# Optimization experiments

Hardware: AMD Instinct MI355X
Metric: run time of the kernel (lower is better)

The kernel has to match this reference:

```python
import jax, jax.numpy as jnp
import numpy as np

B, S_CTX, S_Q, D_CTX, D_Q = 16, 2048, 2048, 1024, 1024
MASK_P = 0.1  # fraction of masked context positions


def setup_inputs() -> dict:
    key = jax.random.key(0)
    k1, k2, k3, k4 = jax.random.split(key, 4)
    context = jax.random.normal(k1, (B, S_CTX, D_CTX), dtype=jnp.float32)
    query = jax.random.normal(k2, (S_Q, B, D_Q), dtype=jnp.float32)  # [q_steps, batch, query_size]
    W = jax.random.normal(k3, (D_CTX, D_Q), dtype=jnp.float32)       # learned bilinear weights
    context_mask = jax.random.uniform(k4, (B, S_CTX)) < MASK_P       # True = masked position
    return {"context": context, "query": query, "W": W, "context_mask": context_mask}


def reference(context, query, W, context_mask):
    # scores[b, q, s] = context[b, s, :] @ W @ query[q, b, :]   (temp = 1.0, so no scaling)
    cw = jnp.einsum('bsd,de->bse', context, W)            # [B, S_ctx, D_q]
    scores = jnp.einsum('bse,qbe->bqs', cw, query)        # [B, S_q, S_ctx]
    neg = jnp.asarray(-1e30, scores.dtype)                # finite stand-in for -inf (NaN-safe)
    scores = jnp.where(context_mask[:, None, :], neg, scores)
    attn = jax.nn.softmax(scores, axis=2)                 # [B, S_q, S_ctx]
    # rows where the whole context is masked get attention zeroed out
    all_masked = jnp.all(context_mask, axis=1)[:, None, None]
    attn = jnp.where(all_masked, jnp.asarray(0.0, attn.dtype), attn)
    composition = jnp.einsum('bqs,bsd->qbd', attn, context)  # [S_q, B, D_ctx]
    attn_out = attn.transpose(1, 0, 2)                       # [S_q, B, S_ctx]
    return attn_out, composition
```

## Files before the change

kernel.cpp:

```cpp
#include <hip/hip_runtime.h>
#include <cmath>

#define B_  16
#define SEQ 2048
#define DIM 1024
#define LDST 40

typedef short  short8 __attribute__((ext_vector_type(8)));
typedef short  sh4    __attribute__((ext_vector_type(4)));
typedef float  f32x4  __attribute__((ext_vector_type(4)));

__device__ __forceinline__ unsigned short f2bf(float x) {
  unsigned u = __builtin_bit_cast(unsigned, x);
  return (unsigned short)((u + 0x7fffu + ((u >> 16) & 1u)) >> 16);
}
__device__ __forceinline__ float bf2f(unsigned short h) {
  unsigned u = ((unsigned)h) << 16;
  return __builtin_bit_cast(float, u);
}

__device__ __forceinline__ void gl16(const void* g, void* l) {
  __builtin_amdgcn_global_load_lds(
      (const __attribute__((address_space(1))) void*)g,
      (__attribute__((address_space(3))) void*)l, 16, 0, 0);
}

__global__ __launch_bounds__(256) void cvt_ctx(const float* __restrict__ X,
                                               unsigned short* __restrict__ hi,
                                               unsigned short* __restrict__ lo) {
  const size_t N8 = (size_t)B_ * SEQ * DIM / 8;
  for (size_t i = (size_t)blockIdx.x * 256 + threadIdx.x; i < N8;
       i += (size_t)gridDim.x * 256) {
    const size_t base = i * 8;
    float4 a = *(const float4*)&X[base];
    float4 c = *(const float4*)&X[base + 4];
    const float xs[8] = {a.x, a.y, a.z, a.w, c.x, c.y, c.z, c.w};
    short8 h, l;
#pragma unroll
    for (int j = 0; j < 8; ++j) {
      unsigned short hh = f2bf(xs[j]);
      h[j] = (short)hh;
      l[j] = (short)f2bf(xs[j] - bf2f(hh));
    }
    *(short8*)&hi[base] = h;
    *(short8*)&lo[base] = l;
  }
}

__global__ __launch_bounds__(256) void t_ctx(const float* __restrict__ X,
                                             unsigned short* __restrict__ T) {
  __shared__ unsigned short L[64 * 72];
  const int t = threadIdx.x;
  const int d0 = blockIdx.x * 64, s0 = blockIdx.y * 64, b = blockIdx.z;
#pragma unroll
  for (int p = 0; p < 4; ++p) {
    const int sl = (t >> 4) + p * 16, d4 = (t & 15) * 4;
    float4 v = *(const float4*)&X[((size_t)b * SEQ + s0 + sl) * DIM + d0 + d4];
    sh4 o = {(short)f2bf(v.x), (short)f2bf(v.y), (short)f2bf(v.z), (short)f2bf(v.w)};
    *(sh4*)&L[sl * 72 + d4] = o;
  }
  __syncthreads();
#pragma unroll
  for (int p = 0; p < 4; ++p) {
    const int dl = (t >> 4) + p * 16, s4 = (t & 15) * 4;
    sh4 o = {(short)L[(s4 + 0) * 72 + dl], (short)L[(s4 + 1) * 72 + dl],
             (short)L[(s4 + 2) * 72 + dl], (short)L[(s4 + 3) * 72 + dl]};
    *(sh4*)&T[((size_t)b * DIM + d0 + dl) * SEQ + s0 + s4] = o;
  }
}

__global__ __launch_bounds__(256) void g1_z(const float* __restrict__ Q,
                                            const float* __restrict__ W,
                                            unsigned short* __restrict__ zhi,
                                            unsigned short* __restrict__ zlo) {
  __shared__ unsigned short Ah[128 * LDST], Al[128 * LDST];
  __shared__ unsigned short Bh[128 * LDST], Bl[128 * LDST];
  const int tid = threadIdx.x;
  const int m0 = blockIdx.y * 128, n0 = blockIdx.x * 128;
  const int wave = tid >> 6, lane = tid & 63;
  const int wm = (wave >> 1) * 64, wn = (wave & 1) * 64;
  const int rl = tid & 127;

  const float* srow = (tid < 128) ? Q + (size_t)(m0 + rl) * DIM
                                  : W + (size_t)(n0 + rl) * DIM;
  unsigned short* th = (tid < 128) ? Ah : Bh;
  unsigned short* tl = (tid < 128) ? Al : Bl;

  f32x4 acc[4][4];
#pragma unroll
  for (int i = 0; i < 4; ++i)
#pragma unroll
    for (int j = 0; j < 4; ++j) acc[i][j] = (f32x4){0.f, 0.f, 0.f, 0.f};

  for (int kc = 0; kc < DIM; kc += 32) {
    float4 fv[8];
#pragma unroll
    for (int j = 0; j < 8; ++j) fv[j] = *(const float4*)&srow[kc + j * 4];
    __syncthreads();
    short8 hv[4], lv[4];
#pragma unroll
    for (int j = 0; j < 8; ++j) {
      const float x[4] = {fv[j].x, fv[j].y, fv[j].z, fv[j].w};
#pragma unroll
      for (int c = 0; c < 4; ++c) {
        unsigned short h = f2bf(x[c]);
        unsigned short l = f2bf(x[c] - bf2f(h));
        hv[j >> 1][(j & 1) * 4 + c] = (short)h;
        lv[j >> 1][(j & 1) * 4 + c] = (short)l;
      }
    }
#pragma unroll
    for (int j = 0; j < 4; ++j) {
      *(short8*)&th[rl * LDST + j * 8] = hv[j];
      *(short8*)&tl[rl * LDST + j * 8] = lv[j];
    }
    __syncthreads();

    short8 ah[4], al[4], bh[4], bl[4];
#pragma unroll
    for (int f = 0; f < 4; ++f) {
      const int ao = (wm + f * 16 + (lane & 15)) * LDST + (lane >> 4) * 8;
      const int bo = (wn + f * 16 + (lane & 15)) * LDST + (lane >> 4) * 8;
      ah[f] = *(const short8*)&Ah[ao];  al[f] = *(const short8*)&Al[ao];
      bh[f] = *(const short8*)&Bh[bo];  bl[f] = *(const short8*)&Bl[bo];
    }
#pragma unroll
    for (int i = 0; i < 4; ++i)
#pragma unroll
      for (int j = 0; j < 4; ++j) {
        acc[i][j] = __builtin_amdgcn_mfma_f32_16x16x32_bf16(ah[i], bh[j], acc[i][j], 0, 0, 0);
        acc[i][j] = __builtin_amdgcn_mfma_f32_16x16x32_bf16(al[i], bh[j], acc[i][j], 0, 0, 0);
        acc[i][j] = __builtin_amdgcn_mfma_f32_16x16x32_bf16(ah[i], bl[j], acc[i][j], 0, 0, 0);
      }
  }
#pragma unroll
  for (int i = 0; i < 4; ++i)
#pragma unroll
    for (int j = 0; j < 4; ++j)
#pragma unroll
      for (int r = 0; r < 4; ++r) {
        const int row = m0 + wm + i * 16 + (lane >> 4) * 4 + r;
        const int col = n0 + wn + j * 16 + (lane & 15);
        const float v = acc[i][j][r];
        const unsigned short h = f2bf(v);
        zhi[(size_t)row * DIM + col] = h;
        zlo[(size_t)row * DIM + col] = f2bf(v - bf2f(h));
      }
}

#define G2GRID (16 * 16 * B_)
__global__ __launch_bounds__(256) void g2_scores(const unsigned short* __restrict__ zhi,
                                                 const unsigned short* __restrict__ zlo,
                                                 const unsigned short* __restrict__ chi,
                                                 const unsigned short* __restrict__ clo,
                                                 float* __restrict__ Sc) {
  __shared__ unsigned short Sh[128 * 32], Sl[128 * 32];
  __shared__ unsigned short Qh[128 * 32], Ql[128 * 32];
  const int tid = threadIdx.x, lane = tid & 63, wave = tid >> 6;

  const int lin = blockIdx.x;
  const int swz = (lin & 7) * (G2GRID / 8) + (lin >> 3);
  const int s0 = (swz & 15) * 128;
  const int q0 = ((swz >> 4) & 15) * 128;
  const int b  = swz >> 8;

  const int wm = (wave >> 1) * 64;
  const int wn = (wave & 1) * 64;

  const int r_sub = lane >> 2;
  const int c_sub = (((lane & 3) ^ ((lane >> 3) & 3))) * 8;

  f32x4 acc[4][4];
#pragma unroll
  for (int i = 0; i < 4; ++i)
#pragma unroll
    for (int j = 0; j < 4; ++j) acc[i][j] = (f32x4){0.f, 0.f, 0.f, 0.f};

  for (int kc = 0; kc < DIM; kc += 32) {
    if (wave == 0) {
#pragma unroll
      for (int it = 0; it < 8; ++it)
        gl16(&chi[((size_t)b * SEQ + s0 + it * 16 + r_sub) * DIM + kc + c_sub], &Sh[it * 512]);
    } else if (wave == 1) {
#pragma unroll
      for (int it = 0; it < 8; ++it)
        gl16(&clo[((size_t)b * SEQ + s0 + it * 16 + r_sub) * DIM + kc + c_sub], &Sl[it * 512]);
    } else if (wave == 2) {
#pragma unroll
      for (int it = 0; it < 8; ++it)
        gl16(&zhi[((size_t)(q0 + it * 16 + r_sub) * B_ + b) * DIM + kc + c_sub], &Qh[it * 512]);
    } else {
#pragma unroll
      for (int it = 0; it < 8; ++it)
        gl16(&zlo[((size_t)(q0 + it * 16 + r_sub) * B_ + b) * DIM + kc + c_sub], &Ql[it * 512]);
    }
    __syncthreads();

    short8 sh_[4], sl_[4], qh_[4], ql_[4];
#pragma unroll
    for (int f = 0; f < 4; ++f) {
      const int ra = wm + f * 16 + (lane & 15);
      const int rb = wn + f * 16 + (lane & 15);
      const int so = ra * 32 + (((lane >> 4) ^ ((ra >> 1) & 3))) * 8;
      const int qo = rb * 32 + (((lane >> 4) ^ ((rb >> 1) & 3))) * 8;
      sh_[f] = *(const short8*)&Sh[so];  sl_[f] = *(const short8*)&Sl[so];
      qh_[f] = *(const short8*)&Qh[qo];  ql_[f] = *(const short8*)&Ql[qo];
    }
#pragma unroll
    for (int i = 0; i < 4; ++i)
#pragma unroll
      for (int j = 0; j < 4; ++j) {
        acc[i][j] = __builtin_amdgcn_mfma_f32_16x16x32_bf16(sh_[i], qh_[j], acc[i][j], 0, 0, 0);
        acc[i][j] = __builtin_amdgcn_mfma_f32_16x16x32_bf16(sl_[i], qh_[j], acc[i][j], 0, 0, 0);
        acc[i][j] = __builtin_amdgcn_mfma_f32_16x16x32_bf16(sh_[i], ql_[j], acc[i][j], 0, 0, 0);
      }
    __syncthreads();
  }

#pragma unroll
  for (int i = 0; i < 4; ++i)
#pragma unroll
    for (int j = 0; j < 4; ++j) {
      const int s = s0 + wm + i * 16 + (lane >> 4) * 4;
      const int q = q0 + wn + j * 16 + (lane & 15);
      f32x4 v = {acc[i][j][0], acc[i][j][1], acc[i][j][2], acc[i][j][3]};
      __builtin_nontemporal_store(v, (f32x4*)&Sc[((size_t)q * B_ + b) * SEQ + s]);
    }
}

__global__ __launch_bounds__(256) void kernel_softmax(float* __restrict__ attn,
                                                      const int* __restrict__ mask) {
  const int row = blockIdx.x;
  const int b = row & (B_ - 1);
  float* p = attn + (size_t)row * SEQ;
  const int* m = mask + (size_t)b * SEQ;
  const int t = threadIdx.x;

  float v[8];
  float mx = -INFINITY;
#pragma unroll
  for (int i = 0; i < 8; ++i) {
    const int s = t + i * 256;
    float x = p[s];
    x = m[s] ? -1e30f : x;
    v[i] = x;
    mx = fmaxf(mx, x);
  }
#pragma unroll
  for (int off = 32; off > 0; off >>= 1) mx = fmaxf(mx, __shfl_xor(mx, off));
  __shared__ float redmax[4];
  __shared__ float redsum[4];
  if ((t & 63) == 0) redmax[t >> 6] = mx;
  __syncthreads();
  mx = fmaxf(fmaxf(redmax[0], redmax[1]), fmaxf(redmax[2], redmax[3]));

  float sum = 0.f;
#pragma unroll
  for (int i = 0; i < 8; ++i) {
    v[i] = __expf(v[i] - mx);
    sum += v[i];
  }
#pragma unroll
  for (int off = 32; off > 0; off >>= 1) sum += __shfl_xor(sum, off);
  if ((t & 63) == 0) redsum[t >> 6] = sum;
  __syncthreads();
  sum = (redsum[0] + redsum[1]) + (redsum[2] + redsum[3]);

  const bool allmasked = (mx < -1e29f);
  const float inv = allmasked ? 0.f : 1.f / sum;
#pragma unroll
  for (int i = 0; i < 8; ++i) p[t + i * 256] = v[i] * inv;
}

__global__ __launch_bounds__(256) void g3_comp(const float* __restrict__ attn,
                                               const unsigned short* __restrict__ ctxT,
                                               float* __restrict__ Out) {
  __shared__ unsigned short Ad[128 * 32];
  __shared__ unsigned short Bq[128 * 32];
  const int tid = threadIdx.x, lane = tid & 63, wave = tid >> 6;
  const int b = blockIdx.z;
  const int d0 = blockIdx.x * 128, q0 = blockIdx.y * 128;
  const int wm = (wave >> 1) * 64;
  const int wn = (wave & 1) * 64;

  const int r_sub = lane >> 2;
  const int c_sub = (((lane & 3) ^ ((lane >> 3) & 3))) * 8;

  const int qrow = tid >> 1, shalf = (tid & 1) * 16;
  const float* arow = attn + ((size_t)(q0 + qrow) * B_ + b) * SEQ;
  const int qsw = (qrow >> 1) & 3;
  const int blk_base = (tid & 1) * 2;
  unsigned short* bdst0 = &Bq[qrow * 32 + ((blk_base + 0) ^ qsw) * 8];
  unsigned short* bdst1 = &Bq[qrow * 32 + ((blk_base + 1) ^ qsw) * 8];

  f32x4 acc[4][4];
#pragma unroll
  for (int i = 0; i < 4; ++i)
#pragma unroll
    for (int j = 0; j < 4; ++j) acc[i][j] = (f32x4){0.f, 0.f, 0.f, 0.f};

  for (int kc = 0; kc < SEQ; kc += 32) {
    float4 fv[4];
#pragma unroll
    for (int j = 0; j < 4; ++j) fv[j] = *(const float4*)&arow[kc + shalf + j * 4];
#pragma unroll
    for (int i = 0; i < 2; ++i) {
      const int rb = wave * 32 + i * 16;
      gl16(&ctxT[((size_t)b * DIM + d0 + rb + r_sub) * SEQ + kc + c_sub], &Ad[rb * 32]);
    }
    short8 bv0, bv1;
#pragma unroll
    for (int j = 0; j < 4; ++j) {
      const float x[4] = {fv[j].x, fv[j].y, fv[j].z, fv[j].w};
#pragma unroll
      for (int c = 0; c < 4; ++c) {
        const int e = j * 4 + c;
        if (e < 8) bv0[e] = (short)f2bf(x[c]);
        else       bv1[e - 8] = (short)f2bf(x[c]);
      }
    }
    *(short8*)bdst0 = bv0;
    *(short8*)bdst1 = bv1;
    __syncthreads();

    short8 af[4], bf_[4];
#pragma unroll
    for (int f = 0; f < 4; ++f) {
      const int ra = wm + f * 16 + (lane & 15);
      const int rb = wn + f * 16 + (lane & 15);
      af[f]  = *(const short8*)&Ad[ra * 32 + (((lane >> 4) ^ ((ra >> 1) & 3))) * 8];
      bf_[f] = *(const short8*)&Bq[rb * 32 + (((lane >> 4) ^ ((rb >> 1) & 3))) * 8];
    }
#pragma unroll
    for (int i = 0; i < 4; ++i)
#pragma unroll
      for (int j = 0; j < 4; ++j)
        acc[i][j] = __builtin_amdgcn_mfma_f32_16x16x32_bf16(af[i], bf_[j], acc[i][j], 0, 0, 0);
    __syncthreads();
  }

#pragma unroll
  for (int i = 0; i < 4; ++i)
#pragma unroll
    for (int j = 0; j < 4; ++j) {
      const int d = d0 + wm + i * 16 + (lane >> 4) * 4;
      const int q = q0 + wn + j * 16 + (lane & 15);
      f32x4 v = {acc[i][j][0], acc[i][j][1], acc[i][j][2], acc[i][j][3]};
      __builtin_nontemporal_store(v, (f32x4*)&Out[((size_t)q * B_ + b) * DIM + d]);
    }
}

extern "C" void kernel_launch(void* const* d_in, const int* in_sizes, int n_in,
                              void* d_out, int out_size, void* d_ws, size_t ws_size,
                              hipStream_t stream) {
  const float* context = (const float*)d_in[0];
  const float* query   = (const float*)d_in[1];
  const float* W       = (const float*)d_in[2];
  const int*   mask    = (const int*)d_in[3];

  float* attn = (float*)d_out;
  float* comp = attn + (size_t)SEQ * B_ * SEQ;

  unsigned short* chi = (unsigned short*)comp;
  unsigned short* clo = chi + (size_t)B_ * SEQ * DIM;

  unsigned short* zhi  = (unsigned short*)d_ws;
  unsigned short* zlo  = zhi + (size_t)SEQ * B_ * DIM;
  unsigned short* ctxT = (unsigned short*)d_ws;

  cvt_ctx<<<dim3(4096), 256, 0, stream>>>(context, chi, clo);
  g1_z<<<dim3(DIM / 128, (SEQ * B_) / 128), 256, 0, stream>>>(query, W, zhi, zlo);
  g2_scores<<<dim3(G2GRID), 256, 0, stream>>>(zhi, zlo, chi, clo, attn);
  t_ctx<<<dim3(DIM / 64, SEQ / 64, B_), 256, 0, stream>>>(context, ctxT);
  kernel_softmax<<<dim3(SEQ * B_), 256, 0, stream>>>(attn, mask);
  g3_comp<<<dim3(DIM / 128, SEQ / 128, B_), 256, 0, stream>>>(attn, ctxT, comp);
}
```

Baseline: 1.258 ms.

## Double-buffer LDS in score and composition GEMMs, vectorize softmax accesses

The g2_scores and g3_comp kernels now use two LDS buffers, so the next K-chunk's global-to-LDS loads (and, in g3_comp, the attention fp32 loads and bf16 conversion) are issued before the MFMAs on the current chunk. This is meant to hide global memory latency behind compute and leaves one barrier per iteration instead of two, with explicit waitcnt and sched_barrier placement. The softmax kernel switches to contiguous float4/int4 loads and stores per thread. The cost is doubled LDS use, which may reduce occupancy, and more hand-managed synchronisation.

```diff
diff --git a/kernel.cpp b/kernel.cpp
--- a/kernel.cpp
+++ b/kernel.cpp
@@ -24,6 +24,11 @@
       (const __attribute__((address_space(1))) void*)g,
       (__attribute__((address_space(3))) void*)l, 16, 0, 0);
 }
+
+#define VMCNT0   asm volatile("s_waitcnt vmcnt(0)" ::: "memory")
+#define LGKMCNT0 asm volatile("s_waitcnt lgkmcnt(0)" ::: "memory")
+#define SCHEDB   __builtin_amdgcn_sched_barrier(0)
+#define SBAR     __builtin_amdgcn_s_barrier()
 
 __global__ __launch_bounds__(256) void cvt_ctx(const float* __restrict__ X,
                                                unsigned short* __restrict__ hi,
@@ -154,8 +159,8 @@
                                                  const unsigned short* __restrict__ chi,
                                                  const unsigned short* __restrict__ clo,
                                                  float* __restrict__ Sc) {
-  __shared__ unsigned short Sh[128 * 32], Sl[128 * 32];
-  __shared__ unsigned short Qh[128 * 32], Ql[128 * 32];
+  __shared__ unsigned short Sh[2][128 * 32], Sl[2][128 * 32];
+  __shared__ unsigned short Qh[2][128 * 32], Ql[2][128 * 32];
   const int tid = threadIdx.x, lane = tid & 63, wave = tid >> 6;
 
   const int lin = blockIdx.x;
@@ -170,32 +175,40 @@
   const int r_sub = lane >> 2;
   const int c_sub = (((lane & 3) ^ ((lane >> 3) & 3))) * 8;
 
+  const unsigned short* plane = (wave == 0) ? chi : (wave == 1) ? clo
+                              : (wave == 2) ? zhi : zlo;
+  const size_t gbase  = (wave < 2) ? ((size_t)b * SEQ + s0) * DIM
+                                   : ((size_t)q0 * B_ + b) * DIM;
+  const size_t gpitch = (wave < 2) ? (size_t)DIM : (size_t)B_ * DIM;
+  const unsigned short* gp = plane + gbase + (size_t)r_sub * gpitch + c_sub;
+  unsigned short* lb[2] = {
+    (wave == 0) ? Sh[0] : (wave == 1) ? Sl[0] : (wave == 2) ? Qh[0] : Ql[0],
+    (wave == 0) ? Sh[1] : (wave == 1) ? Sl[1] : (wave == 2) ? Qh[1] : Ql[1]};
+
+  auto stage = [&](unsigned short* dst, int kc) {
+#pragma unroll
+    for (int it = 0; it < 8; ++it)
+      gl16(gp + (size_t)it * 16 * gpitch + kc, dst + it * 512);
+  };
+
   f32x4 acc[4][4];
 #pragma unroll
   for (int i = 0; i < 4; ++i)
 #pragma unroll
     for (int j = 0; j < 4; ++j) acc[i][j] = (f32x4){0.f, 0.f, 0.f, 0.f};
 
+  stage(lb[0], 0);
+  VMCNT0;
+  SBAR; SCHEDB;
+
+  int cur = 0;
   for (int kc = 0; kc < DIM; kc += 32) {
-    if (wave == 0) {
-#pragma unroll
-      for (int it = 0; it < 8; ++it)
-        gl16(&chi[((size_t)b * SEQ + s0 + it * 16 + r_sub) * DIM + kc + c_sub], &Sh[it * 512]);
-    } else if (wave == 1) {
-#pragma unroll
-      for (int it = 0; it < 8; ++it)
-        gl16(&clo[((size_t)b * SEQ + s0 + it * 16 + r_sub) * DIM + kc + c_sub], &Sl[it * 512]);
-    } else if (wave == 2) {
-#pragma unroll
-      for (int it = 0; it < 8; ++it)
-        gl16(&zhi[((size_t)(q0 + it * 16 + r_sub) * B_ + b) * DIM + kc + c_sub], &Qh[it * 512]);
-    } else {
-#pragma unroll
-      for (int it = 0; it < 8; ++it)
-        gl16(&zlo[((size_t)(q0 + it * 16 + r_sub) * B_ + b) * DIM + kc + c_sub], &Ql[it * 512]);
-    }
-    __syncthreads();
-
+    if (kc + 32 < DIM) stage(lb[cur ^ 1], kc + 32);
+
+    const unsigned short* Shc = Sh[cur];
+    const unsigned short* Slc = Sl[cur];
+    const unsigned short* Qhc = Qh[cur];
+    const unsigned short* Qlc = Ql[cur];
     short8 sh_[4], sl_[4], qh_[4], ql_[4];
 #pragma unroll
     for (int f = 0; f < 4; ++f) {
@@ -203,8 +216,8 @@
       const int rb = wn + f * 16 + (lane & 15);
       const int so = ra * 32 + (((lane >> 4) ^ ((ra >> 1) & 3))) * 8;
       const int qo = rb * 32 + (((lane >> 4) ^ ((rb >> 1) & 3))) * 8;
-      sh_[f] = *(const short8*)&Sh[so];  sl_[f] = *(const short8*)&Sl[so];
-      qh_[f] = *(const short8*)&Qh[qo];  ql_[f] = *(const short8*)&Ql[qo];
+      sh_[f] = *(const short8*)&Shc[so];  sl_[f] = *(const short8*)&Slc[so];
+      qh_[f] = *(const short8*)&Qhc[qo];  ql_[f] = *(const short8*)&Qlc[qo];
     }
 #pragma unroll
     for (int i = 0; i < 4; ++i)
@@ -214,7 +227,9 @@
         acc[i][j] = __builtin_amdgcn_mfma_f32_16x16x32_bf16(sl_[i], qh_[j], acc[i][j], 0, 0, 0);
         acc[i][j] = __builtin_amdgcn_mfma_f32_16x16x32_bf16(sh_[i], ql_[j], acc[i][j], 0, 0, 0);
       }
-    __syncthreads();
+    VMCNT0;
+    SCHEDB; SBAR; SCHEDB;
+    cur ^= 1;
   }
 
 #pragma unroll
@@ -236,16 +251,17 @@
   const int* m = mask + (size_t)b * SEQ;
   const int t = threadIdx.x;
 
-  float v[8];
+  float4 va = *(const float4*)&p[t * 8];
+  float4 vb = *(const float4*)&p[t * 8 + 4];
+  int4 ma = *(const int4*)&m[t * 8];
+  int4 mb = *(const int4*)&m[t * 8 + 4];
+  float v[8] = {ma.x ? -1e30f : va.x, ma.y ? -1e30f : va.y,
+                ma.z ? -1e30f : va.z, ma.w ? -1e30f : va.w,
+                mb.x ? -1e30f : vb.x, mb.y ? -1e30f : vb.y,
+                mb.z ? -1e30f : vb.z, mb.w ? -1e30f : vb.w};
   float mx = -INFINITY;
 #pragma unroll
-  for (int i = 0; i < 8; ++i) {
-    const int s = t + i * 256;
-    float x = p[s];
-    x = m[s] ? -1e30f : x;
-    v[i] = x;
-    mx = fmaxf(mx, x);
-  }
+  for (int i = 0; i < 8; ++i) mx = fmaxf(mx, v[i]);
 #pragma unroll
   for (int off = 32; off > 0; off >>= 1) mx = fmaxf(mx, __shfl_xor(mx, off));
   __shared__ float redmax[4];
@@ -268,15 +284,17 @@
 
   const bool allmasked = (mx < -1e29f);
   const float inv = allmasked ? 0.f : 1.f / sum;
-#pragma unroll
-  for (int i = 0; i < 8; ++i) p[t + i * 256] = v[i] * inv;
+  float4 oa = {v[0] * inv, v[1] * inv, v[2] * inv, v[3] * inv};
+  float4 ob = {v[4] * inv, v[5] * inv, v[6] * inv, v[7] * inv};
+  *(float4*)&p[t * 8] = oa;
+  *(float4*)&p[t * 8 + 4] = ob;
 }
 
 __global__ __launch_bounds__(256) void g3_comp(const float* __restrict__ attn,
                                                const unsigned short* __restrict__ ctxT,
                                                float* __restrict__ Out) {
-  __shared__ unsigned short Ad[128 * 32];
-  __shared__ unsigned short Bq[128 * 32];
+  __shared__ unsigned short Ad[2][128 * 32];
+  __shared__ unsigned short Bq[2][128 * 32];
   const int tid = threadIdx.x, lane = tid & 63, wave = tid >> 6;
   const int b = blockIdx.z;
   const int d0 = blockIdx.x * 128, q0 = blockIdx.y * 128;
@@ -286,12 +304,20 @@
   const int r_sub = lane >> 2;
   const int c_sub = (((lane & 3) ^ ((lane >> 3) & 3))) * 8;
 
+  const unsigned short* agp =
+      ctxT + ((size_t)b * DIM + d0 + wave * 32 + r_sub) * SEQ + c_sub;
+  auto stageA = [&](unsigned short* dst, int kc) {
+#pragma unroll
+    for (int i = 0; i < 2; ++i)
+      gl16(agp + (size_t)i * 16 * SEQ + kc, dst + (wave * 32 + i * 16) * 32);
+  };
+
   const int qrow = tid >> 1, shalf = (tid & 1) * 16;
   const float* arow = attn + ((size_t)(q0 + qrow) * B_ + b) * SEQ;
   const int qsw = (qrow >> 1) & 3;
   const int blk_base = (tid & 1) * 2;
-  unsigned short* bdst0 = &Bq[qrow * 32 + ((blk_base + 0) ^ qsw) * 8];
-  unsigned short* bdst1 = &Bq[qrow * 32 + ((blk_base + 1) ^ qsw) * 8];
+  const int bo0 = qrow * 32 + ((blk_base + 0) ^ qsw) * 8;
+  const int bo1 = qrow * 32 + ((blk_base + 1) ^ qsw) * 8;
 
   f32x4 acc[4][4];
 #pragma unroll
@@ -299,44 +325,75 @@
 #pragma unroll
     for (int j = 0; j < 4; ++j) acc[i][j] = (f32x4){0.f, 0.f, 0.f, 0.f};
 
-  for (int kc = 0; kc < SEQ; kc += 32) {
-    float4 fv[4];
-#pragma unroll
-    for (int j = 0; j < 4; ++j) fv[j] = *(const float4*)&arow[kc + shalf + j * 4];
-#pragma unroll
-    for (int i = 0; i < 2; ++i) {
-      const int rb = wave * 32 + i * 16;
-      gl16(&ctxT[((size_t)b * DIM + d0 + rb + r_sub) * SEQ + kc + c_sub], &Ad[rb * 32]);
-    }
-    short8 bv0, bv1;
+  float4 pv[4];
+#pragma unroll
+  for (int j = 0; j < 4; ++j) pv[j] = *(const float4*)&arow[shalf + j * 4];
+  stageA(Ad[0], 0);
+  VMCNT0;
+  {
+    short8 b0, b1;
 #pragma unroll
     for (int j = 0; j < 4; ++j) {
-      const float x[4] = {fv[j].x, fv[j].y, fv[j].z, fv[j].w};
+      const float x[4] = {pv[j].x, pv[j].y, pv[j].z, pv[j].w};
 #pragma unroll
       for (int c = 0; c < 4; ++c) {
         const int e = j * 4 + c;
-        if (e < 8) bv0[e] = (short)f2bf(x[c]);
-        else       bv1[e - 8] = (short)f2bf(x[c]);
-      }
-    }
-    *(short8*)bdst0 = bv0;
-    *(short8*)bdst1 = bv1;
-    __syncthreads();
-
+        if (e < 8) b0[e] = (short)f2bf(x[c]);
+        else       b1[e - 8] = (short)f2bf(x[c]);
+      }
+    }
+    *(short8*)&Bq[0][bo0] = b0;
+    *(short8*)&Bq[0][bo1] = b1;
+  }
+  LGKMCNT0;
+  SBAR; SCHEDB;
+
+  int cur = 0;
+  for (int kc = 0; kc < SEQ; kc += 32) {
+    const bool more = (kc + 32 < SEQ);
+    float4 nv[4];
+    if (more) {
+#pragma unroll
+      for (int j = 0; j < 4; ++j) nv[j] = *(const float4*)&arow[kc + 32 + shalf + j * 4];
+      stageA(Ad[cur ^ 1], kc + 32);
+    }
+
+    const unsigned short* Adc = Ad[cur];
+    const unsigned short* Bqc = Bq[cur];
     short8 af[4], bf_[4];
 #pragma unroll
     for (int f = 0; f < 4; ++f) {
       const int ra = wm + f * 16 + (lane & 15);
       const int rb = wn + f * 16 + (lane & 15);
-      af[f]  = *(const short8*)&Ad[ra * 32 + (((lane >> 4) ^ ((ra >> 1) & 3))) * 8];
-      bf_[f] = *(const short8*)&Bq[rb * 32 + (((lane >> 4) ^ ((rb >> 1) & 3))) * 8];
+      af[f]  = *(const short8*)&Adc[ra * 32 + (((lane >> 4) ^ ((ra >> 1) & 3))) * 8];
+      bf_[f] = *(const short8*)&Bqc[rb * 32 + (((lane >> 4) ^ ((rb >> 1) & 3))) * 8];
     }
 #pragma unroll
     for (int i = 0; i < 4; ++i)
 #pragma unroll
       for (int j = 0; j < 4; ++j)
         acc[i][j] = __builtin_amdgcn_mfma_f32_16x16x32_bf16(af[i], bf_[j], acc[i][j], 0, 0, 0);
-    __syncthreads();
+
+    VMCNT0;
+    if (more) {
+      short8 b0, b1;
+#pragma unroll
+      for (int j = 0; j < 4; ++j) {
+        const float x[4] = {nv[j].x, nv[j].y, nv[j].z, nv[j].w};
+#pragma unroll
+        for (int c = 0; c < 4; ++c) {
+          const int e = j * 4 + c;
+          if (e < 8) b0[e] = (short)f2bf(x[c]);
+          else       b1[e - 8] = (short)f2bf(x[c]);
+        }
+      }
+      unsigned short* Bqn = Bq[cur ^ 1];
+      *(short8*)&Bqn[bo0] = b0;
+      *(short8*)&Bqn[bo1] = b1;
+    }
+    LGKMCNT0;
+    SCHEDB; SBAR; SCHEDB;
+    cur ^= 1;
   }
 
 #pragma unroll
```

Measured after the change: 1.295 ms. +2.9%, slower.

## Enlarge score and composition GEMM tiles to 256x256 with 8 waves

Applied to the files above, without the earlier changes.

The scores and composition GEMMs move from 128x128 tiles with 4 waves to 256x256 tiles with 8 waves per block. Each wave now computes a 128x64 sub-tile, and the A fragments are loaded per row inside the MFMA loop to hold down register use. The composition grid is linearized and swizzled. The aim is more MFMA work per LDS load and less global traffic per output. The softmax kernel also switches to vectorized float4/int4 loads and stores with contiguous per-thread chunks. The price is higher register pressure (a 32-accumulator array per wave) and fewer, larger blocks, which could hurt occupancy or tail balance.

```diff
diff --git a/kernel.cpp b/kernel.cpp
--- a/kernel.cpp
+++ b/kernel.cpp
@@ -148,77 +148,78 @@
       }
 }
 
-#define G2GRID (16 * 16 * B_)
-__global__ __launch_bounds__(256) void g2_scores(const unsigned short* __restrict__ zhi,
-                                                 const unsigned short* __restrict__ zlo,
-                                                 const unsigned short* __restrict__ chi,
-                                                 const unsigned short* __restrict__ clo,
-                                                 float* __restrict__ Sc) {
-  __shared__ unsigned short Sh[128 * 32], Sl[128 * 32];
-  __shared__ unsigned short Qh[128 * 32], Ql[128 * 32];
+#define G2GRID 1024
+__global__ __launch_bounds__(512, 2) void g2_scores(const unsigned short* __restrict__ zhi,
+                                                    const unsigned short* __restrict__ zlo,
+                                                    const unsigned short* __restrict__ chi,
+                                                    const unsigned short* __restrict__ clo,
+                                                    float* __restrict__ Sc) {
+  __shared__ unsigned short Sh[256 * 32], Sl[256 * 32];
+  __shared__ unsigned short Qh[256 * 32], Ql[256 * 32];
   const int tid = threadIdx.x, lane = tid & 63, wave = tid >> 6;
 
   const int lin = blockIdx.x;
   const int swz = (lin & 7) * (G2GRID / 8) + (lin >> 3);
-  const int s0 = (swz & 15) * 128;
-  const int q0 = ((swz >> 4) & 15) * 128;
-  const int b  = swz >> 8;
-
-  const int wm = (wave >> 1) * 64;
-  const int wn = (wave & 1) * 64;
+  const int b   = swz >> 6;
+  const int tile = swz & 63;
+  const int s0 = (tile >> 3) * 256;
+  const int q0 = (tile & 7) * 256;
+
+  const int wm = (wave >> 2) * 128;
+  const int wn = (wave & 3) * 64;
 
   const int r_sub = lane >> 2;
   const int c_sub = (((lane & 3) ^ ((lane >> 3) & 3))) * 8;
 
-  f32x4 acc[4][4];
-#pragma unroll
-  for (int i = 0; i < 4; ++i)
+  const int plane_id = wave >> 1;
+  const int rowoff   = (wave & 1) * 128;
+  const unsigned short* plane = (plane_id == 0) ? chi : (plane_id == 1) ? clo
+                              : (plane_id == 2) ? zhi : zlo;
+  const size_t gbase  = (plane_id < 2) ? ((size_t)b * SEQ + s0 + rowoff) * DIM
+                                       : ((size_t)(q0 + rowoff) * B_ + b) * DIM;
+  const size_t gpitch = (plane_id < 2) ? (size_t)DIM : (size_t)B_ * DIM;
+  const unsigned short* gp = plane + gbase + (size_t)r_sub * gpitch + c_sub;
+  unsigned short* lbase = ((plane_id == 0) ? Sh : (plane_id == 1) ? Sl
+                         : (plane_id == 2) ? Qh : Ql) + rowoff * 32;
+
+  f32x4 acc[8][4];
+#pragma unroll
+  for (int i = 0; i < 8; ++i)
 #pragma unroll
     for (int j = 0; j < 4; ++j) acc[i][j] = (f32x4){0.f, 0.f, 0.f, 0.f};
 
   for (int kc = 0; kc < DIM; kc += 32) {
-    if (wave == 0) {
-#pragma unroll
-      for (int it = 0; it < 8; ++it)
-        gl16(&chi[((size_t)b * SEQ + s0 + it * 16 + r_sub) * DIM + kc + c_sub], &Sh[it * 512]);
-    } else if (wave == 1) {
-#pragma unroll
-      for (int it = 0; it < 8; ++it)
-        gl16(&clo[((size_t)b * SEQ + s0 + it * 16 + r_sub) * DIM + kc + c_sub], &Sl[it * 512]);
-    } else if (wave == 2) {
-#pragma unroll
-      for (int it = 0; it < 8; ++it)
-        gl16(&zhi[((size_t)(q0 + it * 16 + r_sub) * B_ + b) * DIM + kc + c_sub], &Qh[it * 512]);
-    } else {
-#pragma unroll
-      for (int it = 0; it < 8; ++it)
-        gl16(&zlo[((size_t)(q0 + it * 16 + r_sub) * B_ + b) * DIM + kc + c_sub], &Ql[it * 512]);
-    }
-    __syncthreads();
-
-    short8 sh_[4], sl_[4], qh_[4], ql_[4];
-#pragma unroll
-    for (int f = 0; f < 4; ++f) {
-      const int ra = wm + f * 16 + (lane & 15);
-      const int rb = wn + f * 16 + (lane & 15);
+#pragma unroll
+    for (int it = 0; it < 8; ++it)
+      gl16(gp + (size_t)it * 16 * gpitch + kc, lbase + it * 512);
+    __syncthreads();
+
+    short8 qh_[4], ql_[4];
+#pragma unroll
+    for (int j = 0; j < 4; ++j) {
+      const int rb = wn + j * 16 + (lane & 15);
+      const int qo = rb * 32 + (((lane >> 4) ^ ((rb >> 1) & 3))) * 8;
+      qh_[j] = *(const short8*)&Qh[qo];
+      ql_[j] = *(const short8*)&Ql[qo];
+    }
+#pragma unroll
+    for (int i = 0; i < 8; ++i) {
+      const int ra = wm + i * 16 + (lane & 15);
       const int so = ra * 32 + (((lane >> 4) ^ ((ra >> 1) & 3))) * 8;
-      const int qo = rb * 32 + (((lane >> 4) ^ ((rb >> 1) & 3))) * 8;
-      sh_[f] = *(const short8*)&Sh[so];  sl_[f] = *(const short8*)&Sl[so];
-      qh_[f] = *(const short8*)&Qh[qo];  ql_[f] = *(const short8*)&Ql[qo];
-    }
-#pragma unroll
-    for (int i = 0; i < 4; ++i)
+      const short8 shf = *(const short8*)&Sh[so];
+      const short8 slf = *(const short8*)&Sl[so];
 #pragma unroll
       for (int j = 0; j < 4; ++j) {
-        acc[i][j] = __builtin_amdgcn_mfma_f32_16x16x32_bf16(sh_[i], qh_[j], acc[i][j], 0, 0, 0);
-        acc[i][j] = __builtin_amdgcn_mfma_f32_16x16x32_bf16(sl_[i], qh_[j], acc[i][j], 0, 0, 0);
-        acc[i][j] = __builtin_amdgcn_mfma_f32_16x16x32_bf16(sh_[i], ql_[j], acc[i][j], 0, 0, 0);
-      }
-    __syncthreads();
-  }
-
-#pragma unroll
-  for (int i = 0; i < 4; ++i)
+        acc[i][j] = __builtin_amdgcn_mfma_f32_16x16x32_bf16(shf, qh_[j], acc[i][j], 0, 0, 0);
+        acc[i][j] = __builtin_amdgcn_mfma_f32_16x16x32_bf16(slf, qh_[j], acc[i][j], 0, 0, 0);
+        acc[i][j] = __builtin_amdgcn_mfma_f32_16x16x32_bf16(shf, ql_[j], acc[i][j], 0, 0, 0);
+      }
+    }
+    __syncthreads();
+  }
+
+#pragma unroll
+  for (int i = 0; i < 8; ++i)
 #pragma unroll
     for (int j = 0; j < 4; ++j) {
       const int s = s0 + wm + i * 16 + (lane >> 4) * 4;
@@ -236,16 +237,17 @@
   const int* m = mask + (size_t)b * SEQ;
   const int t = threadIdx.x;
 
-  float v[8];
+  float4 va = *(const float4*)&p[t * 8];
+  float4 vb = *(const float4*)&p[t * 8 + 4];
+  int4 ma = *(const int4*)&m[t * 8];
+  int4 mb = *(const int4*)&m[t * 8 + 4];
+  float v[8] = {ma.x ? -1e30f : va.x, ma.y ? -1e30f : va.y,
+                ma.z ? -1e30f : va.z, ma.w ? -1e30f : va.w,
+                mb.x ? -1e30f : vb.x, mb.y ? -1e30f : vb.y,
+                mb.z ? -1e30f : vb.z, mb.w ? -1e30f : vb.w};
   float mx = -INFINITY;
 #pragma unroll
-  for (int i = 0; i < 8; ++i) {
-    const int s = t + i * 256;
-    float x = p[s];
-    x = m[s] ? -1e30f : x;
-    v[i] = x;
-    mx = fmaxf(mx, x);
-  }
+  for (int i = 0; i < 8; ++i) mx = fmaxf(mx, v[i]);
 #pragma unroll
   for (int off = 32; off > 0; off >>= 1) mx = fmaxf(mx, __shfl_xor(mx, off));
   __shared__ float redmax[4];
@@ -268,34 +270,45 @@
 
   const bool allmasked = (mx < -1e29f);
   const float inv = allmasked ? 0.f : 1.f / sum;
-#pragma unroll
-  for (int i = 0; i < 8; ++i) p[t + i * 256] = v[i] * inv;
-}
-
-__global__ __launch_bounds__(256) void g3_comp(const float* __restrict__ attn,
-                                               const unsigned short* __restrict__ ctxT,
-                                               float* __restrict__ Out) {
-  __shared__ unsigned short Ad[128 * 32];
-  __shared__ unsigned short Bq[128 * 32];
+  float4 oa = {v[0] * inv, v[1] * inv, v[2] * inv, v[3] * inv};
+  float4 ob = {v[4] * inv, v[5] * inv, v[6] * inv, v[7] * inv};
+  *(float4*)&p[t * 8] = oa;
+  *(float4*)&p[t * 8 + 4] = ob;
+}
+
+#define G3GRID 512
+__global__ __launch_bounds__(512, 2) void g3_comp(const float* __restrict__ attn,
+                                                  const unsigned short* __restrict__ ctxT,
+                                                  float* __restrict__ Out) {
+  __shared__ unsigned short Ad[256 * 32];
+  __shared__ unsigned short Bq[256 * 32];
   const int tid = threadIdx.x, lane = tid & 63, wave = tid >> 6;
-  const int b = blockIdx.z;
-  const int d0 = blockIdx.x * 128, q0 = blockIdx.y * 128;
-  const int wm = (wave >> 1) * 64;
-  const int wn = (wave & 1) * 64;
+
+  const int lin = blockIdx.x;
+  const int swz = (lin & 7) * (G3GRID / 8) + (lin >> 3);
+  const int b   = swz >> 5;
+  const int tile = swz & 31;
+  const int d0 = (tile >> 3) * 256;
+  const int q0 = (tile & 7) * 256;
+
+  const int wm = (wave >> 2) * 128;
+  const int wn = (wave & 3) * 64;
 
   const int r_sub = lane >> 2;
   const int c_sub = (((lane & 3) ^ ((lane >> 3) & 3))) * 8;
+
+  const unsigned short* agp =
+      ctxT + ((size_t)b * DIM + d0 + wave * 32 + r_sub) * SEQ + c_sub;
 
   const int qrow = tid >> 1, shalf = (tid & 1) * 16;
   const float* arow = attn + ((size_t)(q0 + qrow) * B_ + b) * SEQ;
   const int qsw = (qrow >> 1) & 3;
-  const int blk_base = (tid & 1) * 2;
-  unsigned short* bdst0 = &Bq[qrow * 32 + ((blk_base + 0) ^ qsw) * 8];
-  unsigned short* bdst1 = &Bq[qrow * 32 + ((blk_base + 1) ^ qsw) * 8];
-
-  f32x4 acc[4][4];
-#pragma unroll
-  for (int i = 0; i < 4; ++i)
+  const int bo0 = qrow * 32 + ((((tid & 1) * 2 + 0)) ^ qsw) * 8;
+  const int bo1 = qrow * 32 + ((((tid & 1) * 2 + 1)) ^ qsw) * 8;
+
+  f32x4 acc[8][4];
+#pragma unroll
+  for (int i = 0; i < 8; ++i)
 #pragma unroll
     for (int j = 0; j < 4; ++j) acc[i][j] = (f32x4){0.f, 0.f, 0.f, 0.f};
 
@@ -303,44 +316,42 @@
     float4 fv[4];
 #pragma unroll
     for (int j = 0; j < 4; ++j) fv[j] = *(const float4*)&arow[kc + shalf + j * 4];
-#pragma unroll
-    for (int i = 0; i < 2; ++i) {
-      const int rb = wave * 32 + i * 16;
-      gl16(&ctxT[((size_t)b * DIM + d0 + rb + r_sub) * SEQ + kc + c_sub], &Ad[rb * 32]);
-    }
-    short8 bv0, bv1;
+    gl16(agp + kc, &Ad[(wave * 32) * 32]);
+    gl16(agp + (size_t)16 * SEQ + kc, &Ad[(wave * 32 + 16) * 32]);
+    short8 b0, b1;
 #pragma unroll
     for (int j = 0; j < 4; ++j) {
       const float x[4] = {fv[j].x, fv[j].y, fv[j].z, fv[j].w};
 #pragma unroll
       for (int c = 0; c < 4; ++c) {
         const int e = j * 4 + c;
-        if (e < 8) bv0[e] = (short)f2bf(x[c]);
-        else       bv1[e - 8] = (short)f2bf(x[c]);
-      }
-    }
-    *(short8*)bdst0 = bv0;
-    *(short8*)bdst1 = bv1;
-    __syncthreads();
-
-    short8 af[4], bf_[4];
-#pragma unroll
-    for (int f = 0; f < 4; ++f) {
-      const int ra = wm + f * 16 + (lane & 15);
-      const int rb = wn + f * 16 + (lane & 15);
-      af[f]  = *(const short8*)&Ad[ra * 32 + (((lane >> 4) ^ ((ra >> 1) & 3))) * 8];
-      bf_[f] = *(const short8*)&Bq[rb * 32 + (((lane >> 4) ^ ((rb >> 1) & 3))) * 8];
-    }
-#pragma unroll
-    for (int i = 0; i < 4; ++i)
+        if (e < 8) b0[e] = (short)f2bf(x[c]);
+        else       b1[e - 8] = (short)f2bf(x[c]);
+      }
+    }
+    *(short8*)&Bq[bo0] = b0;
+    *(short8*)&Bq[bo1] = b1;
+    __syncthreads();
+
+    short8 bf_[4];
+#pragma unroll
+    for (int j = 0; j < 4; ++j) {
+      const int rb = wn + j * 16 + (lane & 15);
+      bf_[j] = *(const short8*)&Bq[rb * 32 + (((lane >> 4) ^ ((rb >> 1) & 3))) * 8];
+    }
+#pragma unroll
+    for (int i = 0; i < 8; ++i) {
+      const int ra = wm + i * 16 + (lane & 15);
+      const short8 af = *(const short8*)&Ad[ra * 32 + (((lane >> 4) ^ ((ra >> 1) & 3))) * 8];
 #pragma unroll
       for (int j = 0; j < 4; ++j)
-        acc[i][j] = __builtin_amdgcn_mfma_f32_16x16x32_bf16(af[i], bf_[j], acc[i][j], 0, 0, 0);
-    __syncthreads();
-  }
-
-#pragma unroll
-  for (int i = 0; i < 4; ++i)
+        acc[i][j] = __builtin_amdgcn_mfma_f32_16x16x32_bf16(af, bf_[j], acc[i][j], 0, 0, 0);
+    }
+    __syncthreads();
+  }
+
+#pragma unroll
+  for (int i = 0; i < 8; ++i)
 #pragma unroll
     for (int j = 0; j < 4; ++j) {
       const int d = d0 + wm + i * 16 + (lane >> 4) * 4;
@@ -370,8 +381,8 @@
 
   cvt_ctx<<<dim3(4096), 256, 0, stream>>>(context, chi, clo);
   g1_z<<<dim3(DIM / 128, (SEQ * B_) / 128), 256, 0, stream>>>(query, W, zhi, zlo);
-  g2_scores<<<dim3(G2GRID), 256, 0, stream>>>(zhi, zlo, chi, clo, attn);
+  g2_scores<<<dim3(G2GRID), 512, 0, stream>>>(zhi, zlo, chi, clo, attn);
   t_ctx<<<dim3(DIM / 64, SEQ / 64, B_), 256, 0, stream>>>(context, ctxT);
   kernel_softmax<<<dim3(SEQ * B_), 256, 0, stream>>>(attn, mask);
-  g3_comp<<<dim3(DIM / 128, SEQ / 128, B_), 256, 0, stream>>>(attn, ctxT, comp);
-}
+  g3_comp<<<dim3(G3GRID), 512, 0, stream>>>(attn, ctxT, comp);
+}
```

Result: slower. 1.464 ms (+16.4%).

## Pipeline score GEMM with 256x256 tiles, double-buffered LDS and interleaved loads

Applied to the files above, without the earlier changes.

The scores GEMM moves from 128x128 tiles with 4 waves to 256x256 tiles with 8 waves. It double-buffers LDS and splits each k-step into four MFMA phases with staggered global-to-LDS loads, explicit waitcnt, barriers and setprio, so memory traffic overlaps compute. The transpose kernel now reads the already-converted bf16 hi plane instead of the fp32 context, and softmax uses contiguous vectorized float4/int4 accesses. The larger tile cuts global reloads but raises register and LDS pressure (128 KB of LDS per block with 2 blocks requested), and the hand-placed waitcnts risk race bugs.

```diff
diff --git a/kernel.cpp b/kernel.cpp
--- a/kernel.cpp
+++ b/kernel.cpp
@@ -24,6 +24,9 @@
       (const __attribute__((address_space(1))) void*)g,
       (__attribute__((address_space(3))) void*)l, 16, 0, 0);
 }
+
+#define SCHEDB __builtin_amdgcn_sched_barrier(0)
+#define SBAR   __builtin_amdgcn_s_barrier()
 
 __global__ __launch_bounds__(256) void cvt_ctx(const float* __restrict__ X,
                                                unsigned short* __restrict__ hi,
@@ -47,26 +50,26 @@
   }
 }
 
-__global__ __launch_bounds__(256) void t_ctx(const float* __restrict__ X,
+__global__ __launch_bounds__(256) void t_chi(const unsigned short* __restrict__ H,
                                              unsigned short* __restrict__ T) {
-  __shared__ unsigned short L[64 * 72];
+  __shared__ unsigned short L[64][72];
   const int t = threadIdx.x;
   const int d0 = blockIdx.x * 64, s0 = blockIdx.y * 64, b = blockIdx.z;
-#pragma unroll
-  for (int p = 0; p < 4; ++p) {
-    const int sl = (t >> 4) + p * 16, d4 = (t & 15) * 4;
-    float4 v = *(const float4*)&X[((size_t)b * SEQ + s0 + sl) * DIM + d0 + d4];
-    sh4 o = {(short)f2bf(v.x), (short)f2bf(v.y), (short)f2bf(v.z), (short)f2bf(v.w)};
-    *(sh4*)&L[sl * 72 + d4] = o;
-  }
+  const int sl = t >> 2, dp = (t & 3) * 16;
+  short8 v0 = *(const short8*)&H[((size_t)b * SEQ + s0 + sl) * DIM + d0 + dp];
+  short8 v1 = *(const short8*)&H[((size_t)b * SEQ + s0 + sl) * DIM + d0 + dp + 8];
+  *(short8*)&L[sl][dp] = v0;
+  *(short8*)&L[sl][dp + 8] = v1;
   __syncthreads();
-#pragma unroll
-  for (int p = 0; p < 4; ++p) {
-    const int dl = (t >> 4) + p * 16, s4 = (t & 15) * 4;
-    sh4 o = {(short)L[(s4 + 0) * 72 + dl], (short)L[(s4 + 1) * 72 + dl],
-             (short)L[(s4 + 2) * 72 + dl], (short)L[(s4 + 3) * 72 + dl]};
-    *(sh4*)&T[((size_t)b * DIM + d0 + dl) * SEQ + s0 + s4] = o;
-  }
+  const int dl = t >> 2, sp = (t & 3) * 16;
+  short8 o0, o1;
+#pragma unroll
+  for (int k = 0; k < 8; ++k) {
+    o0[k] = (short)L[sp + k][dl];
+    o1[k] = (short)L[sp + 8 + k][dl];
+  }
+  *(short8*)&T[((size_t)b * DIM + d0 + dl) * SEQ + s0 + sp] = o0;
+  *(short8*)&T[((size_t)b * DIM + d0 + dl) * SEQ + s0 + sp + 8] = o1;
 }
 
 __global__ __launch_bounds__(256) void g1_z(const float* __restrict__ Q,
@@ -148,77 +151,206 @@
       }
 }
 
-#define G2GRID (16 * 16 * B_)
-__global__ __launch_bounds__(256) void g2_scores(const unsigned short* __restrict__ zhi,
-                                                 const unsigned short* __restrict__ zlo,
-                                                 const unsigned short* __restrict__ chi,
-                                                 const unsigned short* __restrict__ clo,
-                                                 float* __restrict__ Sc) {
-  __shared__ unsigned short Sh[128 * 32], Sl[128 * 32];
-  __shared__ unsigned short Qh[128 * 32], Ql[128 * 32];
+#define G2GRID 1024
+__global__ __launch_bounds__(512, 2) void g2_scores(
+    const unsigned short* __restrict__ zhi, const unsigned short* __restrict__ zlo,
+    const unsigned short* __restrict__ chi, const unsigned short* __restrict__ clo,
+    float* __restrict__ Sc) {
+  __shared__ unsigned short LB[2][4][256 * 32];
   const int tid = threadIdx.x, lane = tid & 63, wave = tid >> 6;
 
   const int lin = blockIdx.x;
   const int swz = (lin & 7) * (G2GRID / 8) + (lin >> 3);
-  const int s0 = (swz & 15) * 128;
-  const int q0 = ((swz >> 4) & 15) * 128;
-  const int b  = swz >> 8;
-
-  const int wm = (wave >> 1) * 64;
-  const int wn = (wave & 1) * 64;
+  const int b = swz >> 6;
+  const int tile = swz & 63;
+  const int s0 = (tile >> 3) * 256, q0 = (tile & 7) * 256;
+
+  const int wm = (wave >> 2) * 128;
+  const int wn = (wave & 3) * 64;
 
   const int r_sub = lane >> 2;
-  const int c_sub = (((lane & 3) ^ ((lane >> 3) & 3))) * 8;
-
-  f32x4 acc[4][4];
-#pragma unroll
-  for (int i = 0; i < 4; ++i)
+  const int c_sub = ((lane & 3) ^ ((lane >> 3) & 3)) * 8;
+
+  const int plane_id = wave >> 1;
+  const int h = wave & 1;
+  const unsigned short* plane = (plane_id == 0) ? chi : (plane_id == 1) ? clo
+                              : (plane_id == 2) ? zhi : zlo;
+  const size_t gbase = (plane_id < 2) ? ((size_t)b * SEQ + s0 + h * 128) * DIM
+                                      : ((size_t)(q0 + h * 128) * B_ + b) * DIM;
+  const size_t gpitch = (plane_id < 2) ? (size_t)DIM : (size_t)B_ * DIM;
+  const unsigned short* gp = plane + gbase + (size_t)r_sub * gpitch + c_sub;
+  const int ldsbase = h * 128 * 32;
+
+  f32x4 acc[8][4];
+#pragma unroll
+  for (int i = 0; i < 8; ++i)
 #pragma unroll
     for (int j = 0; j < 4; ++j) acc[i][j] = (f32x4){0.f, 0.f, 0.f, 0.f};
 
-  for (int kc = 0; kc < DIM; kc += 32) {
-    if (wave == 0) {
-#pragma unroll
-      for (int it = 0; it < 8; ++it)
-        gl16(&chi[((size_t)b * SEQ + s0 + it * 16 + r_sub) * DIM + kc + c_sub], &Sh[it * 512]);
-    } else if (wave == 1) {
-#pragma unroll
-      for (int it = 0; it < 8; ++it)
-        gl16(&clo[((size_t)b * SEQ + s0 + it * 16 + r_sub) * DIM + kc + c_sub], &Sl[it * 512]);
-    } else if (wave == 2) {
-#pragma unroll
-      for (int it = 0; it < 8; ++it)
-        gl16(&zhi[((size_t)(q0 + it * 16 + r_sub) * B_ + b) * DIM + kc + c_sub], &Qh[it * 512]);
-    } else {
-#pragma unroll
-      for (int it = 0; it < 8; ++it)
-        gl16(&zlo[((size_t)(q0 + it * 16 + r_sub) * B_ + b) * DIM + kc + c_sub], &Ql[it * 512]);
-    }
-    __syncthreads();
-
-    short8 sh_[4], sl_[4], qh_[4], ql_[4];
-#pragma unroll
-    for (int f = 0; f < 4; ++f) {
-      const int ra = wm + f * 16 + (lane & 15);
-      const int rb = wn + f * 16 + (lane & 15);
-      const int so = ra * 32 + (((lane >> 4) ^ ((ra >> 1) & 3))) * 8;
-      const int qo = rb * 32 + (((lane >> 4) ^ ((rb >> 1) & 3))) * 8;
-      sh_[f] = *(const short8*)&Sh[so];  sl_[f] = *(const short8*)&Sl[so];
-      qh_[f] = *(const short8*)&Qh[qo];  ql_[f] = *(const short8*)&Ql[qo];
-    }
+  {
+    unsigned short* dst = &LB[0][plane_id][0] + ldsbase;
+#pragma unroll
+    for (int it = 0; it < 8; ++it)
+      gl16(gp + (size_t)it * 16 * gpitch, dst + it * 512);
+  }
+  asm volatile("s_waitcnt vmcnt(0)" ::: "memory");
+  SBAR; SCHEDB;
+
+  short8 ah[4], al[4], qh[4], ql[4];
+  const int aFirst[4] = {0, 2, 4, 6};
+  const int bFirst[4] = {0, 4, 2, 6};
+
+  for (int t = 0; t < 31; ++t) {
+    const unsigned short* Shp = &LB[t & 1][0][0];
+    const unsigned short* Slp = &LB[t & 1][1][0];
+    const unsigned short* Qhp = &LB[t & 1][2][0];
+    const unsigned short* Qlp = &LB[t & 1][3][0];
+    unsigned short* dstP = &LB[(t + 1) & 1][plane_id][0] + ldsbase;
+    const size_t kn = (size_t)(t + 1) * 32;
+
+#pragma unroll
+    for (int i = 0; i < 4; ++i) {
+      const int ra = wm + i * 16 + (lane & 15);
+      const int so = ra * 32 + (((lane >> 4) ^ ((ra >> 1) & 3)) * 8);
+      ah[i] = *(const short8*)&Shp[so];
+      al[i] = *(const short8*)&Slp[so];
+    }
+#pragma unroll
+    for (int j = 0; j < 2; ++j) {
+      const int rb = wn + j * 16 + (lane & 15);
+      const int qo = rb * 32 + (((lane >> 4) ^ ((rb >> 1) & 3)) * 8);
+      qh[j] = *(const short8*)&Qhp[qo];
+      ql[j] = *(const short8*)&Qlp[qo];
+    }
+    {
+      const int i0 = (plane_id >= 2) ? bFirst[0] : aFirst[0];
+      gl16(gp + (size_t)i0 * 16 * gpitch + kn, dstP + i0 * 512);
+      gl16(gp + (size_t)(i0 + 1) * 16 * gpitch + kn, dstP + (i0 + 1) * 512);
+    }
+    asm volatile("s_waitcnt vmcnt(2)" ::: "memory");
+    SBAR; SCHEDB;
+    asm volatile("s_waitcnt lgkmcnt(0)" ::: "memory");
+    SCHEDB;
+    __builtin_amdgcn_s_setprio(1);
 #pragma unroll
     for (int i = 0; i < 4; ++i)
 #pragma unroll
-      for (int j = 0; j < 4; ++j) {
-        acc[i][j] = __builtin_amdgcn_mfma_f32_16x16x32_bf16(sh_[i], qh_[j], acc[i][j], 0, 0, 0);
-        acc[i][j] = __builtin_amdgcn_mfma_f32_16x16x32_bf16(sl_[i], qh_[j], acc[i][j], 0, 0, 0);
-        acc[i][j] = __builtin_amdgcn_mfma_f32_16x16x32_bf16(sh_[i], ql_[j], acc[i][j], 0, 0, 0);
-      }
-    __syncthreads();
-  }
-
-#pragma unroll
-  for (int i = 0; i < 4; ++i)
+      for (int j = 0; j < 2; ++j) {
+        acc[i][j] = __builtin_amdgcn_mfma_f32_16x16x32_bf16(ah[i], qh[j], acc[i][j], 0, 0, 0);
+        acc[i][j] = __builtin_amdgcn_mfma_f32_16x16x32_bf16(al[i], qh[j], acc[i][j], 0, 0, 0);
+        acc[i][j] = __builtin_amdgcn_mfma_f32_16x16x32_bf16(ah[i], ql[j], acc[i][j], 0, 0, 0);
+      }
+    __builtin_amdgcn_s_setprio(0);
+
+#pragma unroll
+    for (int j = 2; j < 4; ++j) {
+      const int rb = wn + j * 16 + (lane & 15);
+      const int qo = rb * 32 + (((lane >> 4) ^ ((rb >> 1) & 3)) * 8);
+      qh[j] = *(const short8*)&Qhp[qo];
+      ql[j] = *(const short8*)&Qlp[qo];
+    }
+    {
+      const int i0 = (plane_id >= 2) ? bFirst[1] : aFirst[1];
+      gl16(gp + (size_t)i0 * 16 * gpitch + kn, dstP + i0 * 512);
+      gl16(gp + (size_t)(i0 + 1) * 16 * gpitch + kn, dstP + (i0 + 1) * 512);
+    }
+    SBAR; SCHEDB;
+    asm volatile("s_waitcnt lgkmcnt(0)" ::: "memory");
+    SCHEDB;
+    __builtin_amdgcn_s_setprio(1);
+#pragma unroll
+    for (int i = 0; i < 4; ++i)
+#pragma unroll
+      for (int j = 2; j < 4; ++j) {
+        acc[i][j] = __builtin_amdgcn_mfma_f32_16x16x32_bf16(ah[i], qh[j], acc[i][j], 0, 0, 0);
+        acc[i][j] = __builtin_amdgcn_mfma_f32_16x16x32_bf16(al[i], qh[j], acc[i][j], 0, 0, 0);
+        acc[i][j] = __builtin_amdgcn_mfma_f32_16x16x32_bf16(ah[i], ql[j], acc[i][j], 0, 0, 0);
+      }
+    __builtin_amdgcn_s_setprio(0);
+
+#pragma unroll
+    for (int i = 0; i < 4; ++i) {
+      const int ra = wm + (i + 4) * 16 + (lane & 15);
+      const int so = ra * 32 + (((lane >> 4) ^ ((ra >> 1) & 3)) * 8);
+      ah[i] = *(const short8*)&Shp[so];
+      al[i] = *(const short8*)&Slp[so];
+    }
+    {
+      const int i0 = (plane_id >= 2) ? bFirst[2] : aFirst[2];
+      gl16(gp + (size_t)i0 * 16 * gpitch + kn, dstP + i0 * 512);
+      gl16(gp + (size_t)(i0 + 1) * 16 * gpitch + kn, dstP + (i0 + 1) * 512);
+    }
+    SBAR; SCHEDB;
+    asm volatile("s_waitcnt lgkmcnt(0)" ::: "memory");
+    SCHEDB;
+    __builtin_amdgcn_s_setprio(1);
+#pragma unroll
+    for (int i = 0; i < 4; ++i)
+#pragma unroll
+      for (int j = 0; j < 2; ++j) {
+        acc[i + 4][j] = __builtin_amdgcn_mfma_f32_16x16x32_bf16(ah[i], qh[j], acc[i + 4][j], 0, 0, 0);
+        acc[i + 4][j] = __builtin_amdgcn_mfma_f32_16x16x32_bf16(al[i], qh[j], acc[i + 4][j], 0, 0, 0);
+        acc[i + 4][j] = __builtin_amdgcn_mfma_f32_16x16x32_bf16(ah[i], ql[j], acc[i + 4][j], 0, 0, 0);
+      }
+    __builtin_amdgcn_s_setprio(0);
+
+    {
+      const int i0 = (plane_id >= 2) ? bFirst[3] : aFirst[3];
+      gl16(gp + (size_t)i0 * 16 * gpitch + kn, dstP + i0 * 512);
+      gl16(gp + (size_t)(i0 + 1) * 16 * gpitch + kn, dstP + (i0 + 1) * 512);
+    }
+    asm volatile("s_waitcnt vmcnt(4)" ::: "memory");
+    SBAR; SCHEDB;
+    __builtin_amdgcn_s_setprio(1);
+#pragma unroll
+    for (int i = 0; i < 4; ++i)
+#pragma unroll
+      for (int j = 2; j < 4; ++j) {
+        acc[i + 4][j] = __builtin_amdgcn_mfma_f32_16x16x32_bf16(ah[i], qh[j], acc[i + 4][j], 0, 0, 0);
+        acc[i + 4][j] = __builtin_amdgcn_mfma_f32_16x16x32_bf16(al[i], qh[j], acc[i + 4][j], 0, 0, 0);
+        acc[i + 4][j] = __builtin_amdgcn_mfma_f32_16x16x32_bf16(ah[i], ql[j], acc[i + 4][j], 0, 0, 0);
+      }
+    __builtin_amdgcn_s_setprio(0);
+  }
+
+  asm volatile("s_waitcnt vmcnt(0)" ::: "memory");
+  SBAR; SCHEDB;
+  {
+    const unsigned short* Shp = &LB[1][0][0];
+    const unsigned short* Slp = &LB[1][1][0];
+    const unsigned short* Qhp = &LB[1][2][0];
+    const unsigned short* Qlp = &LB[1][3][0];
+#pragma unroll
+    for (int j = 0; j < 4; ++j) {
+      const int rb = wn + j * 16 + (lane & 15);
+      const int qo = rb * 32 + (((lane >> 4) ^ ((rb >> 1) & 3)) * 8);
+      qh[j] = *(const short8*)&Qhp[qo];
+      ql[j] = *(const short8*)&Qlp[qo];
+    }
+#pragma unroll
+    for (int half = 0; half < 2; ++half) {
+#pragma unroll
+      for (int i = 0; i < 4; ++i) {
+        const int ra = wm + (half * 4 + i) * 16 + (lane & 15);
+        const int so = ra * 32 + (((lane >> 4) ^ ((ra >> 1) & 3)) * 8);
+        ah[i] = *(const short8*)&Shp[so];
+        al[i] = *(const short8*)&Slp[so];
+      }
+      asm volatile("s_waitcnt lgkmcnt(0)" ::: "memory");
+      SCHEDB;
+#pragma unroll
+      for (int i = 0; i < 4; ++i)
+#pragma unroll
+        for (int j = 0; j < 4; ++j) {
+          acc[half * 4 + i][j] = __builtin_amdgcn_mfma_f32_16x16x32_bf16(ah[i], qh[j], acc[half * 4 + i][j], 0, 0, 0);
+          acc[half * 4 + i][j] = __builtin_amdgcn_mfma_f32_16x16x32_bf16(al[i], qh[j], acc[half * 4 + i][j], 0, 0, 0);
+          acc[half * 4 + i][j] = __builtin_amdgcn_mfma_f32_16x16x32_bf16(ah[i], ql[j], acc[half * 4 + i][j], 0, 0, 0);
+        }
+    }
+  }
+
+#pragma unroll
+  for (int i = 0; i < 8; ++i)
 #pragma unroll
     for (int j = 0; j < 4; ++j) {
       const int s = s0 + wm + i * 16 + (lane >> 4) * 4;
@@ -236,16 +368,17 @@
   const int* m = mask + (size_t)b * SEQ;
   const int t = threadIdx.x;
 
-  float v[8];
+  float4 va = *(const float4*)&p[t * 8];
+  float4 vb = *(const float4*)&p[t * 8 + 4];
+  int4 ma = *(const int4*)&m[t * 8];
+  int4 mb = *(const int4*)&m[t * 8 + 4];
+  float v[8] = {ma.x ? -1e30f : va.x, ma.y ? -1e30f : va.y,
+                ma.z ? -1e30f : va.z, ma.w ? -1e30f : va.w,
+                mb.x ? -1e30f : vb.x, mb.y ? -1e30f : vb.y,
+                mb.z ? -1e30f : vb.z, mb.w ? -1e30f : vb.w};
   float mx = -INFINITY;
 #pragma unroll
-  for (int i = 0; i < 8; ++i) {
-    const int s = t + i * 256;
-    float x = p[s];
-    x = m[s] ? -1e30f : x;
-    v[i] = x;
-    mx = fmaxf(mx, x);
-  }
+  for (int i = 0; i < 8; ++i) mx = fmaxf(mx, v[i]);
 #pragma unroll
   for (int off = 32; off > 0; off >>= 1) mx = fmaxf(mx, __shfl_xor(mx, off));
   __shared__ float redmax[4];
@@ -268,8 +401,10 @@
 
   const bool allmasked = (mx < -1e29f);
   const float inv = allmasked ? 0.f : 1.f / sum;
-#pragma unroll
-  for (int i = 0; i < 8; ++i) p[t + i * 256] = v[i] * inv;
+  float4 oa = {v[0] * inv, v[1] * inv, v[2] * inv, v[3] * inv};
+  float4 ob = {v[4] * inv, v[5] * inv, v[6] * inv, v[7] * inv};
+  *(float4*)&p[t * 8] = oa;
+  *(float4*)&p[t * 8 + 4] = ob;
 }
 
 __global__ __launch_bounds__(256) void g3_comp(const float* __restrict__ attn,
@@ -286,6 +421,9 @@
   const int r_sub = lane >> 2;
   const int c_sub = (((lane & 3) ^ ((lane >> 3) & 3))) * 8;
 
+  const unsigned short* agp =
+      ctxT + ((size_t)b * DIM + d0 + wave * 32 + r_sub) * SEQ + c_sub;
+
   const int qrow = tid >> 1, shalf = (tid & 1) * 16;
   const float* arow = attn + ((size_t)(q0 + qrow) * B_ + b) * SEQ;
   const int qsw = (qrow >> 1) & 3;
@@ -306,7 +444,7 @@
 #pragma unroll
     for (int i = 0; i < 2; ++i) {
       const int rb = wave * 32 + i * 16;
-      gl16(&ctxT[((size_t)b * DIM + d0 + rb + r_sub) * SEQ + kc + c_sub], &Ad[rb * 32]);
+      gl16(agp + (size_t)i * 16 * SEQ + kc, &Ad[rb * 32]);
     }
     short8 bv0, bv1;
 #pragma unroll
@@ -370,8 +508,8 @@
 
   cvt_ctx<<<dim3(4096), 256, 0, stream>>>(context, chi, clo);
   g1_z<<<dim3(DIM / 128, (SEQ * B_) / 128), 256, 0, stream>>>(query, W, zhi, zlo);
-  g2_scores<<<dim3(G2GRID), 256, 0, stream>>>(zhi, zlo, chi, clo, attn);
-  t_ctx<<<dim3(DIM / 64, SEQ / 64, B_), 256, 0, stream>>>(context, ctxT);
+  g2_scores<<<dim3(G2GRID), 512, 0, stream>>>(zhi, zlo, chi, clo, attn);
+  t_chi<<<dim3(DIM / 64, SEQ / 64, B_), 256, 0, stream>>>(chi, ctxT);
   kernel_softmax<<<dim3(SEQ * B_), 256, 0, stream>>>(attn, mask);
   g3_comp<<<dim3(DIM / 128, SEQ / 128, B_), 256, 0, stream>>>(attn, ctxT, comp);
 }
```

After: 1.396 ms. 11.0% more time.
